# Kernel tuning notes

Hardware: AMD Instinct MI355X
Metric: run time of the kernel (lower is better)

Reference implementation:

```python
import jax, jax.numpy as jnp
import numpy as np

T, B, H, D_MODEL = 4096, 16, 256, 256


def setup_inputs() -> dict:
    key = jax.random.key(0)
    ks = jax.random.split(key, 10)
    x = jax.random.normal(ks[0], (T, B, D_MODEL), jnp.float32)
    # episode-start (reset) flags, sparse
    starts = jax.random.bernoulli(ks[1], 0.005, (T, B, 1))
    state_re = jnp.zeros((1, B, H), jnp.float32)
    state_im = jnp.zeros((1, B, H), jnp.float32)
    # LRU parameterization: |Lambda| = exp(-exp(nu_log)) < 1 for any real nu_log
    nu_log = jax.random.uniform(ks[2], (H,), jnp.float32)
    theta_log = jax.random.uniform(ks[3], (H,), jnp.float32) * 2.0
    s_in = 1.0 / np.sqrt(D_MODEL).astype(np.float32)
    B_re = jax.random.normal(ks[4], (H, D_MODEL), jnp.float32) * s_in
    B_im = jax.random.normal(ks[5], (H, D_MODEL), jnp.float32) * s_in
    s_out = 1.0 / np.sqrt(H).astype(np.float32)
    C_re = jax.random.normal(ks[6], (D_MODEL, H), jnp.float32) * s_out
    C_im = jax.random.normal(ks[7], (D_MODEL, H), jnp.float32) * s_out
    D = jax.random.normal(ks[8], (D_MODEL,), jnp.float32)
    return dict(x=x, starts=starts, state_re=state_re, state_im=state_im,
                nu_log=nu_log, theta_log=theta_log, B_re=B_re, B_im=B_im,
                C_re=C_re, C_im=C_im, D=D)


def _cell_binary_op(lhs, rhs):
    # Resettable diagonal linear-recurrence combine (associative).
    (A_i, b_i), d_i = lhs
    (A_j, b_j), d_j = rhs
    A = jnp.where(d_j, A_j, A_j * A_i)
    b = jnp.where(d_j, b_j, A_j * b_i + b_j)
    return (A, b), jnp.logical_or(d_i, d_j)


def reference(x, starts, state_re, state_im, nu_log, theta_log,
              B_re, B_im, C_re, C_im, D):
    t, b = x.shape[0], x.shape[1]
    # cell.map_to_h
    Lam = jnp.exp(-jnp.exp(nu_log) + 1j * jnp.exp(theta_log))          # [H] complex
    gamma = jnp.sqrt(jnp.clip(1.0 - jnp.abs(Lam) ** 2, 1e-8))          # [H]
    Bu = (jnp.einsum('tbd,hd->tbh', x, B_re * gamma[:, None])
          + 1j * jnp.einsum('tbd,hd->tbh', x, B_im * gamma[:, None]))  # [T,B,H] c64
    Lam_el = jnp.broadcast_to(Lam, (t, b, H)).astype(jnp.complex64)

    # recurrent_associative_scan: prepend carry, scan, drop first element
    A0 = jnp.ones((1, b, H), jnp.complex64)
    b0 = (state_re + 1j * state_im).astype(jnp.complex64)
    d0 = jnp.zeros((1, b, 1), bool)
    A_all = jnp.concatenate([A0, Lam_el], axis=0)
    b_all = jnp.concatenate([b0, Bu], axis=0)
    d_all = jnp.concatenate([d0, starts], axis=0)
    (A_s, b_s), _ = jax.lax.associative_scan(
        _cell_binary_op, ((A_all, b_all), d_all), axis=0)
    h = b_s[1:]                                                        # [T,B,H] c64

    # cell.map_from_h: y = Re(C h) + D * x
    out = (jnp.einsum('tbh,dh->tbd', h.real, C_re)
           - jnp.einsum('tbh,dh->tbd', h.imag, C_im)
           + D * x)
    return out
```

## Files before the change

### kernel.cpp

```cpp
#include <hip/hip_runtime.h>
#include <hip/hip_bf16.h>

#define T_LEN 4096
#define BATCH 16
#define NH    256
#define DM    256
#define M_TOT (T_LEN * BATCH)

typedef __hip_bfloat16 bf16;
typedef __attribute__((ext_vector_type(8))) short bf16x8;
typedef __attribute__((ext_vector_type(4))) float f32x4;

__device__ __forceinline__ unsigned short f2bf_bits(float f) {
    unsigned int u = __float_as_uint(f);
    return (unsigned short)((u + 0x7fffu + ((u >> 16) & 1u)) >> 16);
}

typedef const unsigned int __attribute__((address_space(1)))* gas_ptr;
typedef unsigned int __attribute__((address_space(3)))* las_ptr;
__device__ __forceinline__ void async16(const bf16* g, bf16* l) {
    __builtin_amdgcn_global_load_lds((gas_ptr)g, (las_ptr)l, 16, 0, 0);
}

__global__ __launch_bounds__(256) void prep_lam_kernel(
    const float* __restrict__ nu_log, const float* __restrict__ theta_log,
    float* __restrict__ lam)
{
    int h = threadIdx.x;
    float mod = expf(-expf(nu_log[h]));
    float ang = expf(theta_log[h]);
    lam[h]      = mod * cosf(ang);
    lam[NH + h] = mod * sinf(ang);
}

__global__ __launch_bounds__(256) void prep_w_kernel(
    const float* __restrict__ nu_log,
    const float* __restrict__ B_re, const float* __restrict__ B_im,
    const float* __restrict__ C_re, const float* __restrict__ C_im,
    bf16* __restrict__ WaT, bf16* __restrict__ WcT)
{
    int idx = blockIdx.x * 256 + threadIdx.x;
    if (idx < 512 * 256) {
        int n = idx >> 8, k = idx & 255;
        int h = n >> 1;
        float mod = expf(-expf(nu_log[h]));
        float gam = sqrtf(fmaxf(1.0f - mod * mod, 1e-8f));
        float v = ((n & 1) == 0 ? B_re[h * DM + k] : B_im[h * DM + k]) * gam;
        WaT[idx] = __float2bfloat16(v);
    } else {
        int j = idx - 512 * 256;
        int d = j >> 9, k = j & 511;
        int h = k >> 1;
        float v = ((k & 1) == 0) ? C_re[d * NH + h] : -C_im[d * NH + h];
        WcT[j] = __float2bfloat16(v);
    }
}

__global__ __launch_bounds__(256) void cvt_kernel(
    const float* __restrict__ x, bf16* __restrict__ xb)
{
    size_t i = ((size_t)blockIdx.x * 256 + threadIdx.x) * 8;
    float4 a = *(const float4*)(x + i);
    float4 b = *(const float4*)(x + i + 4);
    union { bf16 h[8]; int4 v; } u;
    u.h[0] = __float2bfloat16(a.x); u.h[1] = __float2bfloat16(a.y);
    u.h[2] = __float2bfloat16(a.z); u.h[3] = __float2bfloat16(a.w);
    u.h[4] = __float2bfloat16(b.x); u.h[5] = __float2bfloat16(b.y);
    u.h[6] = __float2bfloat16(b.z); u.h[7] = __float2bfloat16(b.w);
    *(int4*)(xb + i) = u.v;
}

__global__ __launch_bounds__(256) void gemm_a_kernel(
    const bf16* __restrict__ A,
    const bf16* __restrict__ BT,
    bf16* __restrict__ Cb)
{
    __shared__ bf16 sA[128 * 32];
    __shared__ bf16 sB[128 * 32];

    const int tid  = threadIdx.x;
    const int lane = tid & 63;
    const int wid  = tid >> 6;

    const int bid = blockIdx.x;
    const int xcd = bid & 7;
    const int sl  = bid >> 3;
    const int nt  = sl & 3;
    const int mt  = xcd * 64 + (sl >> 2);
    const int m0  = mt * 128;
    const int n0  = nt * 128;

    const int tm  = (wid >> 1) * 64;
    const int tn  = (wid & 1) * 64;
    const int l15 = lane & 15;
    const int q   = lane >> 4;

    const bf16* gA = A  + (size_t)(m0 + wid * 32 + (lane >> 2)) * 256 + (lane & 3) * 8;
    const bf16* gB = BT + (size_t)(n0 + wid * 32 + (lane >> 2)) * 256 + (lane & 3) * 8;
    const size_t rstep = (size_t)16 * 256;
    bf16* lA = sA + wid * 32 * 32;
    bf16* lB = sB + wid * 32 * 32;

    f32x4 acc[4][4];
    #pragma unroll
    for (int i = 0; i < 4; ++i)
        #pragma unroll
        for (int j = 0; j < 4; ++j) acc[i][j] = (f32x4){0.f, 0.f, 0.f, 0.f};

    for (int k0 = 0; k0 < 256; k0 += 32) {
        async16(gA,         lA);
        async16(gA + rstep, lA + 16 * 32);
        async16(gB,         lB);
        async16(gB + rstep, lB + 16 * 32);
        gA += 32; gB += 32;
        __syncthreads();

        bf16x8 af[4], bfr[4];
        #pragma unroll
        for (int i = 0; i < 4; ++i) {
            af[i]  = *(const bf16x8*)&sA[(tm + i * 16 + l15) * 32 + q * 8];
            bfr[i] = *(const bf16x8*)&sB[(tn + i * 16 + l15) * 32 + q * 8];
        }
        #pragma unroll
        for (int i = 0; i < 4; ++i)
            #pragma unroll
            for (int j = 0; j < 4; ++j)
                acc[i][j] = __builtin_amdgcn_mfma_f32_16x16x32_bf16(
                    af[i], bfr[j], acc[i][j], 0, 0, 0);
        __syncthreads();
    }

    #pragma unroll
    for (int j = 0; j < 4; ++j) {
        int col = n0 + tn + j * 16 + l15;
        #pragma unroll
        for (int i = 0; i < 4; ++i) {
            #pragma unroll
            for (int r = 0; r < 4; ++r) {
                int row = m0 + tm + i * 16 + q * 4 + r;
                Cb[(size_t)row * 512 + col] = __float2bfloat16(acc[i][j][r]);
            }
        }
    }
}

#define SC  32
#define HL  16
#define LDH 520
#define PF  8

__global__ __launch_bounds__(256) void scan_gemmc_kernel(
    const bf16* __restrict__ Bu,
    const bf16* __restrict__ WcT,
    const float* __restrict__ lam,
    const int* __restrict__ starts,
    const float* __restrict__ state_re, const float* __restrict__ state_im,
    const float* __restrict__ x,
    const float* __restrict__ Dvec,
    float* __restrict__ out)
{
    __shared__ bf16 sH[SC * LDH];
    __shared__ bf16 sB[256 * 32];
    __shared__ int  sStarts[SC + HL];

    const int tid = threadIdx.x;
    const int b   = blockIdx.x & (BATCH - 1);
    const int c   = blockIdx.x / BATCH;
    const int t0  = c * SC;
    const int tstart = (c == 0) ? 0 : t0 - HL;
    const int nIter  = t0 + SC - tstart;

    if (tid < nIter) sStarts[tid] = starts[(tstart + tid) * BATCH + b];

    const int h = tid;
    float lr = lam[h], li = lam[NH + h];
    float hre = 0.0f, him = 0.0f;
    if (c == 0) { hre = state_re[b * NH + h]; him = state_im[b * NH + h]; }

    const bf16* bp = Bu + ((size_t)tstart * BATCH + b) * 512 + 2 * h;
    const size_t tstride = (size_t)BATCH * 512;

    unsigned int vbuf[PF];
    #pragma unroll
    for (int p = 0; p < PF; ++p)
        vbuf[p] = (p < nIter) ? *(const unsigned int*)(bp + p * tstride) : 0u;

    __syncthreads();

    const int skip = nIter - SC;
    for (int base = 0; base < nIter; base += PF) {
        #pragma unroll
        for (int p = 0; p < PF; ++p) {
            int it = base + p;
            unsigned int v = vbuf[p];
            int tp = it + PF;
            if (tp < nIter)
                vbuf[p] = *(const unsigned int*)(bp + (size_t)tp * tstride);
            float br = __uint_as_float(v << 16);
            float bi = __uint_as_float(v & 0xffff0000u);
            int st = sStarts[it];
            float nr = st ? br : fmaf(lr, hre, fmaf(-li, him, br));
            float ni = st ? bi : fmaf(lr, him, fmaf(li, hre, bi));
            hre = nr; him = ni;
            int tl = it - skip;
            if (tl >= 0) {
                unsigned int packed =
                    ((unsigned int)f2bf_bits(him) << 16) | f2bf_bits(hre);
                *(unsigned int*)&sH[tl * LDH + 2 * h] = packed;
            }
        }
    }
    __syncthreads();

    const int lane = tid & 63;
    const int w    = tid >> 6;
    const int l15  = lane & 15;
    const int q    = lane >> 4;

    f32x4 acc[2][4];
    #pragma unroll
    for (int i = 0; i < 2; ++i)
        #pragma unroll
        for (int j = 0; j < 4; ++j) acc[i][j] = (f32x4){0.f, 0.f, 0.f, 0.f};

    const bf16* gB = WcT + (size_t)(w * 64 + (lane >> 2)) * 512 + (lane & 3) * 8;
    bf16* lB = sB + w * 64 * 32;

    for (int k0 = 0; k0 < 512; k0 += 32) {
        async16(gB,              lB);
        async16(gB + 16 * 512,   lB + 16 * 32);
        async16(gB + 32 * 512,   lB + 32 * 32);
        async16(gB + 48 * 512,   lB + 48 * 32);
        gB += 32;
        __syncthreads();

        bf16x8 af[2], bfr[4];
        #pragma unroll
        for (int i = 0; i < 2; ++i)
            af[i] = *(const bf16x8*)&sH[(i * 16 + l15) * LDH + k0 + q * 8];
        #pragma unroll
        for (int j = 0; j < 4; ++j)
            bfr[j] = *(const bf16x8*)&sB[(w * 64 + j * 16 + l15) * 32 + q * 8];
        #pragma unroll
        for (int i = 0; i < 2; ++i)
            #pragma unroll
            for (int j = 0; j < 4; ++j)
                acc[i][j] = __builtin_amdgcn_mfma_f32_16x16x32_bf16(
                    af[i], bfr[j], acc[i][j], 0, 0, 0);
        __syncthreads();
    }

    #pragma unroll
    for (int j = 0; j < 4; ++j) {
        int col = w * 64 + j * 16 + l15;
        float dv = Dvec[col];
        #pragma unroll
        for (int i = 0; i < 2; ++i) {
            #pragma unroll
            for (int r = 0; r < 4; ++r) {
                int tl = i * 16 + q * 4 + r;
                size_t m = (size_t)(t0 + tl) * BATCH + b;
                out[m * 256 + col] = acc[i][j][r] + dv * x[m * 256 + col];
            }
        }
    }
}

extern "C" void kernel_launch(void* const* d_in, const int* in_sizes, int n_in,
                              void* d_out, int out_size, void* d_ws, size_t ws_size,
                              hipStream_t stream)
{
    const float* x         = (const float*)d_in[0];
    const int*   starts    = (const int*)d_in[1];
    const float* state_re  = (const float*)d_in[2];
    const float* state_im  = (const float*)d_in[3];
    const float* nu_log    = (const float*)d_in[4];
    const float* theta_log = (const float*)d_in[5];
    const float* B_re      = (const float*)d_in[6];
    const float* B_im      = (const float*)d_in[7];
    const float* C_re      = (const float*)d_in[8];
    const float* C_im      = (const float*)d_in[9];
    const float* Dvec      = (const float*)d_in[10];
    float* out = (float*)d_out;

    char* ws = (char*)d_ws;
    float* lam = (float*)ws;
    bf16*  WaT = (bf16*)(ws + 4096);
    bf16*  WcT = (bf16*)(ws + 4096 + 512 * 256 * 2);
    bf16*  Bu  = (bf16*)(ws + (1 << 20));
    bf16*  xb  = (bf16*)d_out;

    prep_lam_kernel<<<1, 256, 0, stream>>>(nu_log, theta_log, lam);
    prep_w_kernel<<<1024, 256, 0, stream>>>(nu_log, B_re, B_im, C_re, C_im, WaT, WcT);
    cvt_kernel<<<M_TOT * DM / (256 * 8), 256, 0, stream>>>(x, xb);

    gemm_a_kernel<<<2048, 256, 0, stream>>>(xb, WaT, Bu);

    scan_gemmc_kernel<<<(T_LEN / SC) * BATCH, 256, 0, stream>>>(
        Bu, WcT, lam, starts, state_re, state_im, x, Dvec, out);
}
```

Measured before the change: 242.5 us.

## Fuse fp32-to-bf16 conversion into input GEMM and double-buffer weight tiles

```diff
diff --git a/kernel.cpp b/kernel.cpp
--- a/kernel.cpp
+++ b/kernel.cpp
@@ -14,6 +14,15 @@
 __device__ __forceinline__ unsigned short f2bf_bits(float f) {
     unsigned int u = __float_as_uint(f);
     return (unsigned short)((u + 0x7fffu + ((u >> 16) & 1u)) >> 16);
+}
+
+__device__ __forceinline__ bf16x8 cvt8(float4 a, float4 b) {
+    union { unsigned short s[8]; bf16x8 v; } u;
+    u.s[0] = f2bf_bits(a.x); u.s[1] = f2bf_bits(a.y);
+    u.s[2] = f2bf_bits(a.z); u.s[3] = f2bf_bits(a.w);
+    u.s[4] = f2bf_bits(b.x); u.s[5] = f2bf_bits(b.y);
+    u.s[6] = f2bf_bits(b.z); u.s[7] = f2bf_bits(b.w);
+    return u.v;
 }
 
 typedef const unsigned int __attribute__((address_space(1)))* gas_ptr;
@@ -56,27 +65,12 @@
     }
 }
 
-__global__ __launch_bounds__(256) void cvt_kernel(
-    const float* __restrict__ x, bf16* __restrict__ xb)
-{
-    size_t i = ((size_t)blockIdx.x * 256 + threadIdx.x) * 8;
-    float4 a = *(const float4*)(x + i);
-    float4 b = *(const float4*)(x + i + 4);
-    union { bf16 h[8]; int4 v; } u;
-    u.h[0] = __float2bfloat16(a.x); u.h[1] = __float2bfloat16(a.y);
-    u.h[2] = __float2bfloat16(a.z); u.h[3] = __float2bfloat16(a.w);
-    u.h[4] = __float2bfloat16(b.x); u.h[5] = __float2bfloat16(b.y);
-    u.h[6] = __float2bfloat16(b.z); u.h[7] = __float2bfloat16(b.w);
-    *(int4*)(xb + i) = u.v;
-}
-
 __global__ __launch_bounds__(256) void gemm_a_kernel(
-    const bf16* __restrict__ A,
+    const float* __restrict__ x,
     const bf16* __restrict__ BT,
     bf16* __restrict__ Cb)
 {
-    __shared__ bf16 sA[128 * 32];
-    __shared__ bf16 sB[128 * 32];
+    __shared__ bf16 sB[2 * 128 * 32];
 
     const int tid  = threadIdx.x;
     const int lane = tid & 63;
@@ -95,11 +89,9 @@
     const int l15 = lane & 15;
     const int q   = lane >> 4;
 
-    const bf16* gA = A  + (size_t)(m0 + wid * 32 + (lane >> 2)) * 256 + (lane & 3) * 8;
-    const bf16* gB = BT + (size_t)(n0 + wid * 32 + (lane >> 2)) * 256 + (lane & 3) * 8;
+    const bf16* gB0 = BT + (size_t)(n0 + wid * 32 + (lane >> 2)) * 256 + (lane & 3) * 8;
     const size_t rstep = (size_t)16 * 256;
-    bf16* lA = sA + wid * 32 * 32;
-    bf16* lB = sB + wid * 32 * 32;
+    const float* gA = x + (size_t)(m0 + tm + l15) * 256 + q * 8;
 
     f32x4 acc[4][4];
     #pragma unroll
@@ -107,27 +99,43 @@
         #pragma unroll
         for (int j = 0; j < 4; ++j) acc[i][j] = (f32x4){0.f, 0.f, 0.f, 0.f};
 
-    for (int k0 = 0; k0 < 256; k0 += 32) {
-        async16(gA,         lA);
-        async16(gA + rstep, lA + 16 * 32);
-        async16(gB,         lB);
-        async16(gB + rstep, lB + 16 * 32);
-        gA += 32; gB += 32;
+    {
+        bf16* l = sB + wid * 32 * 32;
+        async16(gB0, l);
+        async16(gB0 + rstep, l + 16 * 32);
+    }
+
+    for (int p = 0; p < 8; ++p) {
         __syncthreads();
-
+        if (p < 7) {
+            const bf16* g = gB0 + (p + 1) * 32;
+            bf16* l = sB + ((p + 1) & 1) * (128 * 32) + wid * 32 * 32;
+            async16(g, l);
+            async16(g + rstep, l + 16 * 32);
+        }
+
+        const float* ga = gA + p * 32;
+        float4 va[4][2];
+        #pragma unroll
+        for (int i = 0; i < 4; ++i) {
+            va[i][0] = *(const float4*)(ga + (size_t)i * 16 * 256);
+            va[i][1] = *(const float4*)(ga + (size_t)i * 16 * 256 + 4);
+        }
         bf16x8 af[4], bfr[4];
         #pragma unroll
-        for (int i = 0; i < 4; ++i) {
-            af[i]  = *(const bf16x8*)&sA[(tm + i * 16 + l15) * 32 + q * 8];
-            bfr[i] = *(const bf16x8*)&sB[(tn + i * 16 + l15) * 32 + q * 8];
-        }
+        for (int i = 0; i < 4; ++i) af[i] = cvt8(va[i][0], va[i][1]);
+
+        const bf16* sbp = sB + (p & 1) * (128 * 32);
+        #pragma unroll
+        for (int j = 0; j < 4; ++j)
+            bfr[j] = *(const bf16x8*)&sbp[(tn + j * 16 + l15) * 32 + q * 8];
+
         #pragma unroll
         for (int i = 0; i < 4; ++i)
             #pragma unroll
             for (int j = 0; j < 4; ++j)
                 acc[i][j] = __builtin_amdgcn_mfma_f32_16x16x32_bf16(
                     af[i], bfr[j], acc[i][j], 0, 0, 0);
-        __syncthreads();
     }
 
     #pragma unroll
@@ -147,7 +155,7 @@
 #define SC  32
 #define HL  16
 #define LDH 520
-#define PF  8
+#define PF  16
 
 __global__ __launch_bounds__(256) void scan_gemmc_kernel(
     const bf16* __restrict__ Bu,
@@ -160,8 +168,7 @@
     float* __restrict__ out)
 {
     __shared__ bf16 sH[SC * LDH];
-    __shared__ bf16 sB[256 * 32];
-    __shared__ int  sStarts[SC + HL];
+    __shared__ bf16 sB[2 * 256 * 32];
 
     const int tid = threadIdx.x;
     const int b   = blockIdx.x & (BATCH - 1);
@@ -170,7 +177,19 @@
     const int tstart = (c == 0) ? 0 : t0 - HL;
     const int nIter  = t0 + SC - tstart;
 
-    if (tid < nIter) sStarts[tid] = starts[(tstart + tid) * BATCH + b];
+    const int lane = tid & 63;
+    const int w    = tid >> 6;
+    const int l15  = lane & 15;
+    const int q    = lane >> 4;
+
+    const bf16* gB0 = WcT + (size_t)(w * 64 + (lane >> 2)) * 512 + (lane & 3) * 8;
+    {
+        bf16* l = sB + w * 64 * 32;
+        async16(gB0,            l);
+        async16(gB0 + 16 * 512, l + 16 * 32);
+        async16(gB0 + 32 * 512, l + 32 * 32);
+        async16(gB0 + 48 * 512, l + 48 * 32);
+    }
 
     const int h = tid;
     float lr = lam[h], li = lam[NH + h];
@@ -178,14 +197,16 @@
     if (c == 0) { hre = state_re[b * NH + h]; him = state_im[b * NH + h]; }
 
     const bf16* bp = Bu + ((size_t)tstart * BATCH + b) * 512 + 2 * h;
+    const int* stp = starts + tstart * BATCH + b;
     const size_t tstride = (size_t)BATCH * 512;
 
     unsigned int vbuf[PF];
-    #pragma unroll
-    for (int p = 0; p < PF; ++p)
-        vbuf[p] = (p < nIter) ? *(const unsigned int*)(bp + p * tstride) : 0u;
-
-    __syncthreads();
+    int stbuf[PF];
+    #pragma unroll
+    for (int p = 0; p < PF; ++p) {
+        vbuf[p]  = *(const unsigned int*)(bp + (size_t)p * tstride);
+        stbuf[p] = stp[p * BATCH];
+    }
 
     const int skip = nIter - SC;
     for (int base = 0; base < nIter; base += PF) {
@@ -193,12 +214,14 @@
         for (int p = 0; p < PF; ++p) {
             int it = base + p;
             unsigned int v = vbuf[p];
+            int st = stbuf[p];
             int tp = it + PF;
-            if (tp < nIter)
-                vbuf[p] = *(const unsigned int*)(bp + (size_t)tp * tstride);
+            if (tp < nIter) {
+                vbuf[p]  = *(const unsigned int*)(bp + (size_t)tp * tstride);
+                stbuf[p] = stp[tp * BATCH];
+            }
             float br = __uint_as_float(v << 16);
             float bi = __uint_as_float(v & 0xffff0000u);
-            int st = sStarts[it];
             float nr = st ? br : fmaf(lr, hre, fmaf(-li, him, br));
             float ni = st ? bi : fmaf(lr, him, fmaf(li, hre, bi));
             hre = nr; him = ni;
@@ -210,12 +233,6 @@
             }
         }
     }
-    __syncthreads();
-
-    const int lane = tid & 63;
-    const int w    = tid >> 6;
-    const int l15  = lane & 15;
-    const int q    = lane >> 4;
 
     f32x4 acc[2][4];
     #pragma unroll
@@ -223,31 +240,31 @@
         #pragma unroll
         for (int j = 0; j < 4; ++j) acc[i][j] = (f32x4){0.f, 0.f, 0.f, 0.f};
 
-    const bf16* gB = WcT + (size_t)(w * 64 + (lane >> 2)) * 512 + (lane & 3) * 8;
-    bf16* lB = sB + w * 64 * 32;
-
-    for (int k0 = 0; k0 < 512; k0 += 32) {
-        async16(gB,              lB);
-        async16(gB + 16 * 512,   lB + 16 * 32);
-        async16(gB + 32 * 512,   lB + 32 * 32);
-        async16(gB + 48 * 512,   lB + 48 * 32);
-        gB += 32;
+    for (int p = 0; p < 16; ++p) {
         __syncthreads();
-
+        if (p < 15) {
+            const bf16* g = gB0 + (p + 1) * 32;
+            bf16* l = sB + ((p + 1) & 1) * (256 * 32) + w * 64 * 32;
+            async16(g,            l);
+            async16(g + 16 * 512, l + 16 * 32);
+            async16(g + 32 * 512, l + 32 * 32);
+            async16(g + 48 * 512, l + 48 * 32);
+        }
+
+        const bf16* sbp = sB + (p & 1) * (256 * 32);
         bf16x8 af[2], bfr[4];
         #pragma unroll
         for (int i = 0; i < 2; ++i)
-            af[i] = *(const bf16x8*)&sH[(i * 16 + l15) * LDH + k0 + q * 8];
+            af[i] = *(const bf16x8*)&sH[(i * 16 + l15) * LDH + p * 32 + q * 8];
         #pragma unroll
         for (int j = 0; j < 4; ++j)
-            bfr[j] = *(const bf16x8*)&sB[(w * 64 + j * 16 + l15) * 32 + q * 8];
+            bfr[j] = *(const bf16x8*)&sbp[(w * 64 + j * 16 + l15) * 32 + q * 8];
         #pragma unroll
         for (int i = 0; i < 2; ++i)
             #pragma unroll
             for (int j = 0; j < 4; ++j)
                 acc[i][j] = __builtin_amdgcn_mfma_f32_16x16x32_bf16(
                     af[i], bfr[j], acc[i][j], 0, 0, 0);
-        __syncthreads();
     }
 
     #pragma unroll
@@ -288,13 +305,11 @@
     bf16*  WaT = (bf16*)(ws + 4096);
     bf16*  WcT = (bf16*)(ws + 4096 + 512 * 256 * 2);
     bf16*  Bu  = (bf16*)(ws + (1 << 20));
-    bf16*  xb  = (bf16*)d_out;
 
     prep_lam_kernel<<<1, 256, 0, stream>>>(nu_log, theta_log, lam);
     prep_w_kernel<<<1024, 256, 0, stream>>>(nu_log, B_re, B_im, C_re, C_im, WaT, WcT);
-    cvt_kernel<<<M_TOT * DM / (256 * 8), 256, 0, stream>>>(x, xb);
-
-    gemm_a_kernel<<<2048, 256, 0, stream>>>(xb, WaT, Bu);
+
+    gemm_a_kernel<<<2048, 256, 0, stream>>>(x, WaT, Bu);
 
     scan_gemmc_kernel<<<(T_LEN / SC) * BATCH, 256, 0, stream>>>(
         Bu, WcT, lam, starts, state_re, state_im, x, Dvec, out);
```

Result: slower. 288.8 us (+19.1%).
